# Optimization experiments

Hardware: AMD Instinct MI355X
Metric: run time of the kernel (lower is better)

The kernel has to match this reference:

```python
import jax, jax.numpy as jnp
import numpy as np

N_HEAD = 16


def setup_inputs() -> dict:
    key = jax.random.key(0)
    ks = jax.random.split(key, 10)
    B, S, D = 4, 2048, 1024
    inp = {
        "x": jax.random.normal(ks[0], (B, S, D), dtype=jnp.float32),
        "attention_mask": jnp.ones((B, S), dtype=jnp.int32),
        "Wq": jax.random.normal(ks[1], (D, D), dtype=jnp.float32) * 0.02,
        "bq": jax.random.normal(ks[2], (D,), dtype=jnp.float32) * 0.02,
        "Wk": jax.random.normal(ks[3], (D, D), dtype=jnp.float32) * 0.02,
        "bk": jax.random.normal(ks[4], (D,), dtype=jnp.float32) * 0.02,
        "Wv": jax.random.normal(ks[5], (D, D), dtype=jnp.float32) * 0.02,
        "bv": jax.random.normal(ks[6], (D,), dtype=jnp.float32) * 0.02,
        "Wp": jax.random.normal(ks[7], (D, D), dtype=jnp.float32) * 0.02,
        "bp": jax.random.normal(ks[8], (D,), dtype=jnp.float32) * 0.02,
    }
    return inp


def reference(x, attention_mask, Wq, bq, Wk, bk, Wv, bv, Wp, bp):
    B, S, D = x.shape
    H = N_HEAD
    HD = D // H
    scale = 1.0 / jnp.sqrt(jnp.asarray(HD, dtype=x.dtype))

    # q, kT, v projections -> (B, H, S, HD)
    q = (x @ Wq + bq).reshape(B, S, H, HD).transpose(0, 2, 1, 3)
    k = (x @ Wk + bk).reshape(B, S, H, HD).transpose(0, 2, 1, 3)
    v = (x @ Wv + bv).reshape(B, S, H, HD).transpose(0, 2, 1, 3)

    # scaled scores (B, H, S, S); dropout is identity at inference (p=0)
    logits = jnp.einsum("bhqd,bhkd->bhqk", q, k) * scale

    causal = jnp.tril(jnp.ones((S, S), dtype=bool))
    mask = causal[None, None, :, :] & attention_mask.astype(bool)[:, None, None, :]
    logits = jnp.where(mask, logits, -jnp.inf)

    attn_weights = jax.nn.softmax(logits, axis=-1)
    attn_weights = jnp.nan_to_num(attn_weights)  # fully-masked rows -> 0

    attn = jnp.einsum("bhqk,bhkd->bhqd", attn_weights, v)
    attn = attn.transpose(0, 2, 1, 3).reshape(B, S, D)  # (b h s hd) -> (b s D)
    return attn @ Wp + bp
```

## Files before the change

### kernel.cpp

```cpp
#include <hip/hip_runtime.h>
#include <stdint.h>

typedef __attribute__((ext_vector_type(8))) __bf16 bf16x8;
typedef __attribute__((ext_vector_type(4))) float f32x4;
typedef __attribute__((ext_vector_type(16))) float f32x16;
typedef __attribute__((ext_vector_type(8))) unsigned short u16x8;
typedef __attribute__((ext_vector_type(4))) unsigned int u32x4;
typedef unsigned short u16;

#define S_LEN 2048
#define DM 1024
#define NH 16
#define HD 64
#define BATCH 4

#define SWZ(r, b) ((b) ^ (((r)&7) << 4))

__device__ __forceinline__ int swz64(int row, int c16) {
  return ((row >> 1) << 7) + (((((row & 1) << 2) + c16) ^ ((row >> 1) & 7)) << 4);
}

__device__ __forceinline__ u16 f2b(float f) {
  union { float f; unsigned u; } v; v.f = f;
  unsigned u = v.u;
  u += 0x7fffu + ((u >> 16) & 1u);
  return (u16)(u >> 16);
}

__device__ __forceinline__ void gload_lds16(const void* g, void* l) {
  __builtin_amdgcn_global_load_lds((const __attribute__((address_space(1))) char*)g,
                                   (__attribute__((address_space(3))) char*)l, 16, 0, 0);
}


__global__ void cvt_x_kernel(const float* __restrict__ in, u16* __restrict__ out) {
  const int i = (blockIdx.x * 256 + threadIdx.x) * 8;
  const float4 a = *(const float4*)(in + i);
  const float4 b = *(const float4*)(in + i + 4);
  u16x8 o;
  o[0] = f2b(a.x); o[1] = f2b(a.y); o[2] = f2b(a.z); o[3] = f2b(a.w);
  o[4] = f2b(b.x); o[5] = f2b(b.y); o[6] = f2b(b.z); o[7] = f2b(b.w);
  *(u16x8*)(out + i) = o;
}

__global__ void transpose_cvt_w4_kernel(const float* __restrict__ Wq, const float* __restrict__ Wk,
                                        const float* __restrict__ Wv, const float* __restrict__ Wp,
                                        u16* __restrict__ WtQKV, u16* __restrict__ Wpt) {
  __shared__ float tile[64][65];
  const int z = blockIdx.z;
  const float* W = (z == 0) ? Wq : (z == 1) ? Wk : (z == 2) ? Wv : Wp;
  u16* Wt = (z == 3) ? Wpt : WtQKV + (size_t)z * 1048576;
  const int bx = blockIdx.x, by = blockIdx.y;
  const int t = threadIdx.x;
  const int r = t >> 6, c = t & 63;
#pragma unroll
  for (int i = 0; i < 64; i += 4)
    tile[r + i][c] = W[(size_t)(by * 64 + r + i) * DM + bx * 64 + c];
  __syncthreads();
#pragma unroll
  for (int i = 0; i < 64; i += 4)
    Wt[(size_t)(bx * 64 + r + i) * DM + by * 64 + c] = f2b(tile[c][r + i]);
}

__global__ void transpose_v_kernel(const u16* __restrict__ V, u16* __restrict__ Vt) {
  __shared__ u16 tile[64][68];
  const int st = blockIdx.x, bh = blockIdx.y;
  const int t = threadIdx.x;
  const int r = t >> 6, c = t & 63;
  const u16* src = V + ((size_t)bh * S_LEN + st * 64) * HD;
#pragma unroll
  for (int i = 0; i < 64; i += 4)
    tile[r + i][c] = src[(r + i) * HD + c];
  __syncthreads();
  u16* dst = Vt + (size_t)bh * HD * S_LEN + st * 64;
#pragma unroll
  for (int i = 0; i < 64; i += 4)
    dst[(size_t)(r + i) * S_LEN + c] = tile[c][r + i];
}


__device__ __forceinline__ void gemm_core_128(const u16* __restrict__ Atile,
                                              const u16* __restrict__ Btile,
                                              const int K, u16* As, u16* Bs,
                                              f32x4 acc[4][4]) {
  const int t = threadIdx.x;
  const int wave = t >> 6, lane = t & 63;
  const int wr = wave >> 1, wc = wave & 1;
  const int lr = lane & 15, lg = lane >> 4;

  for (int kt = 0; kt < K; kt += 32) {
#pragma unroll
    for (int i = 0; i < 2; ++i) {
      const int chunk = i * 4 + wave;
      const int off = chunk * 1024 + lane * 16;
      const int row = off >> 6;
      const int colb = off & 63;
      gload_lds16((const char*)Atile + ((size_t)row * K + kt) * 2 + colb,
                  (char*)As + chunk * 1024);
      gload_lds16((const char*)Btile + ((size_t)row * K + kt) * 2 + colb,
                  (char*)Bs + chunk * 1024);
    }
    __syncthreads();
    bf16x8 af[4], bfr[4];
#pragma unroll
    for (int m = 0; m < 4; ++m)
      af[m] = *(const bf16x8*)&As[(wr * 64 + m * 16 + lr) * 32 + lg * 8];
#pragma unroll
    for (int n = 0; n < 4; ++n)
      bfr[n] = *(const bf16x8*)&Bs[(wc * 64 + n * 16 + lr) * 32 + lg * 8];
#pragma unroll
    for (int m = 0; m < 4; ++m)
#pragma unroll
      for (int n = 0; n < 4; ++n)
        acc[m][n] = __builtin_amdgcn_mfma_f32_16x16x32_bf16(af[m], bfr[n], acc[m][n], 0, 0, 0);
    __syncthreads();
  }
}


__global__ __launch_bounds__(512, 2) void gemm_qkv_kernel(
    const u16* __restrict__ xb, const u16* __restrict__ Wt,
    const float* __restrict__ bq, const float* __restrict__ bk, const float* __restrict__ bv,
    u16* __restrict__ Qb, u16* __restrict__ Kb, u16* __restrict__ Vb) {
  __shared__ alignas(16) char L[4][40960];

  const int bcol = (blockIdx.x & 7) * 384;
  const int brow = (blockIdx.x >> 3) * 256;

  const int t = threadIdx.x;
  const int wave = t >> 6, lane = t & 63;
  const int wr = wave >> 2, wc = wave & 3;
  const int lr = lane & 15, lg = lane >> 4;

  f32x4 acc[8][6];
  const f32x4 zf = {0.f, 0.f, 0.f, 0.f};
#pragma unroll
  for (int m = 0; m < 8; ++m)
#pragma unroll
    for (int n = 0; n < 6; ++n) acc[m][n] = zf;

  const char* const Ag = (const char*)xb + (size_t)brow * 2048;
  const char* const Bg = (const char*)Wt + (size_t)bcol * 2048;

  int srcA0, srcA1, srcB0, srcB1, srcB2;
  {
    auto inv = [&](int p) {
      const int rp = p >> 7, slot = (p >> 4) & 7;
      const int v = slot ^ (rp & 7);
      const int row = rp * 2 + (v >> 2), c16 = v & 3;
      return row * 2048 + c16 * 16;
    };
    srcA0 = inv(t * 16);
    srcA1 = inv(8192 + t * 16);
    srcB0 = inv(t * 16);
    srcB1 = inv(8192 + t * 16);
    srcB2 = inv(16384 + t * 16);
  }

  const int aoff0 = swz64(wr * 128 + lr, lg);
  const int boff0 = swz64(wc * 96 + lr, lg);

  auto stage = [&](int kt, int b) {
    char* const base = &L[b][0];
    const int ko = kt * 64;
    gload_lds16(Ag + srcA0 + ko, base + t * 16);
    gload_lds16(Ag + srcA1 + ko, base + 8192 + t * 16);
    gload_lds16(Bg + srcB0 + ko, base + 16384 + t * 16);
    gload_lds16(Bg + srcB1 + ko, base + 24576 + t * 16);
    gload_lds16(Bg + srcB2 + ko, base + 32768 + t * 16);
  };

  const int NT = 32;
  stage(0, 0);
  stage(1, 1);
  for (int kt = 0; kt < NT; ++kt) {
    if (kt + 2 < NT) {
      stage(kt + 2, (kt + 2) & 3);
      asm volatile("s_waitcnt vmcnt(5)" ::: "memory");
    } else if (kt + 1 < NT) {
      asm volatile("s_waitcnt vmcnt(5)" ::: "memory");
    } else {
      asm volatile("s_waitcnt vmcnt(0)" ::: "memory");
    }
    asm volatile("s_barrier" ::: "memory");

    const char* const la = &L[kt & 3][0];
    const char* const lb = la + 16384;
    bf16x8 bf[6];
#pragma unroll
    for (int n = 0; n < 6; ++n) bf[n] = *(const bf16x8*)(lb + boff0 + n * 1024);
    __builtin_amdgcn_s_setprio(1);
#pragma unroll
    for (int m = 0; m < 8; ++m) {
      const bf16x8 af = *(const bf16x8*)(la + aoff0 + m * 1024);
#pragma unroll
      for (int n = 0; n < 6; ++n)
        acc[m][n] = __builtin_amdgcn_mfma_f32_16x16x32_bf16(af, bf[n], acc[m][n], 0, 0, 0);
    }
    __builtin_amdgcn_s_setprio(0);
  }

  const float qsc = 0.18033688011112042f;
#pragma unroll
  for (int m = 0; m < 8; ++m)
#pragma unroll
    for (int n = 0; n < 6; ++n) {
      const int colg = bcol + wc * 96 + n * 16 + lr;
      const int which = colg >> 10;
      const int c1 = colg & 1023;
      const float bias = (which == 0) ? bq[c1] : (which == 1) ? bk[c1] : bv[c1];
      u16* const dst = (which == 0) ? Qb : (which == 1) ? Kb : Vb;
#pragma unroll
      for (int j = 0; j < 4; ++j) {
        const int grow = brow + wr * 128 + m * 16 + lg * 4 + j;
        float val = acc[m][n][j] + bias;
        if (which == 0) val *= qsc;
        const int b = grow >> 11, s = grow & 2047;
        dst[(((size_t)b * NH + (c1 >> 6)) * S_LEN + s) * HD + (c1 & 63)] = f2b(val);
      }
    }
}

__global__ __launch_bounds__(256, 2) void gemm_out_kernel(
    const u16* __restrict__ A, const u16* __restrict__ Bt,
    const float* __restrict__ bias, float* __restrict__ out) {
  __shared__ alignas(16) u16 As[128 * 32], Bs[128 * 32];
  const int brow = blockIdx.x * 128;
  const int bcol = blockIdx.y * 128;
  f32x4 acc[4][4];
  const f32x4 zf = {0.f, 0.f, 0.f, 0.f};
#pragma unroll
  for (int m = 0; m < 4; ++m)
#pragma unroll
    for (int n = 0; n < 4; ++n) acc[m][n] = zf;

  gemm_core_128(A + (size_t)brow * DM, Bt + (size_t)bcol * DM, DM, As, Bs, acc);

  const int t = threadIdx.x, wave = t >> 6, lane = t & 63;
  const int wr = wave >> 1, wc = wave & 1, lr = lane & 15, lg = lane >> 4;
#pragma unroll
  for (int m = 0; m < 4; ++m)
#pragma unroll
    for (int n = 0; n < 4; ++n)
#pragma unroll
      for (int j = 0; j < 4; ++j) {
        const int grow = brow + wr * 64 + m * 16 + lg * 4 + j;
        const int col = bcol + wc * 64 + n * 16 + lr;
        out[(size_t)grow * DM + col] = acc[m][n][j] + bias[col];
      }
}


__global__ __launch_bounds__(256, 4) void flash2_kernel(
    const u16* __restrict__ Qb, const u16* __restrict__ Kb,
    const u16* __restrict__ Vt, u16* __restrict__ attn) {
  __shared__ alignas(16) u16 Ks[2][64 * 64];
  __shared__ alignas(16) u16 Vs[2][64 * 64];
  __shared__ float lbb[4][32];

  const int idx = blockIdx.x;
  const int c = idx & 255, r = idx >> 8;
  const int bh = (c & 15) * 4 + r;
  const int u = c >> 4;
  int qt;
  switch (r) {
    case 0: qt = u; break;
    case 1: qt = 15 - u; break;
    case 2: qt = (u + 8) & 15; break;
    default: qt = (7 - u) & 15; break;
  }

  const int t = threadIdx.x, wave = t >> 6, lane = t & 63;
  const int l31 = lane & 31, hi = lane >> 5;
  const int swz0 = (l31 & 7) << 4;
  const int b = bh >> 4, h = bh & 15;

  const char* kb0 = (const char*)(Kb + (size_t)bh * S_LEN * HD);
  const char* vb0 = (const char*)(Vt + (size_t)bh * HD * S_LEN);

  auto stage = [&](int kt, int bsel) {
#pragma unroll
    for (int i = 0; i < 2; ++i) {
      const int chunk = i * 4 + wave;
      const int off = chunk * 1024 + lane * 16;
      const int row = off >> 7, colb = off & 127;
      gload_lds16(kb0 + (size_t)kt * 8192 + row * 128 + SWZ(row, colb),
                  (char*)Ks[bsel] + chunk * 1024);
      gload_lds16(vb0 + (size_t)row * 4096 + kt * 128 + SWZ(row, colb),
                  (char*)Vs[bsel] + chunk * 1024);
    }
  };

  const int wq = qt * 128 + wave * 32;
  const int myq = wq + l31;

  const u16* qrow = Qb + ((size_t)bh * S_LEN + myq) * HD;
  bf16x8 qf[4];
#pragma unroll
  for (int ks = 0; ks < 4; ++ks)
    qf[ks] = *(const bf16x8*)(qrow + ks * 16 + hi * 8);

  f32x16 oa0, oa1;
#pragma unroll
  for (int r2 = 0; r2 < 16; ++r2) { oa0[r2] = 0.f; oa1[r2] = 0.f; }
  float lsum = 0.f;

  const int last = 2 * qt + 1;
  const int wlast = 2 * qt + (wave >> 1);

  stage(0, 0);
  int cur = 0;
  for (int kt = 0; kt <= last; ++kt) {
    __syncthreads();
    if (kt < last) stage(kt + 1, cur ^ 1);
    if (kt <= wlast) {
      f32x16 s0, s1;
#pragma unroll
      for (int r2 = 0; r2 < 16; ++r2) { s0[r2] = 0.f; s1[r2] = 0.f; }
      const char* ksb = (const char*)Ks[cur];
      __builtin_amdgcn_s_setprio(1);
#pragma unroll
      for (int ks = 0; ks < 4; ++ks) {
        const int byte0 = 32 * ks + 16 * hi;
        const bf16x8 ka = *(const bf16x8*)(ksb + l31 * 128 + (byte0 ^ swz0));
        const bf16x8 kb2 = *(const bf16x8*)(ksb + (32 + l31) * 128 + (byte0 ^ swz0));
        s0 = __builtin_amdgcn_mfma_f32_32x32x16_bf16(ka, qf[ks], s0, 0, 0, 0);
        s1 = __builtin_amdgcn_mfma_f32_32x32x16_bf16(kb2, qf[ks], s1, 0, 0, 0);
      }
      __builtin_amdgcn_s_setprio(0);

      if (kt == wlast) {
        const int kb4 = kt * 64 + 4 * hi;
#pragma unroll
        for (int r2 = 0; r2 < 16; ++r2) {
          const int key = kb4 + (r2 & 3) + 8 * (r2 >> 2);
          if (key > myq) s0[r2] = -1e30f;
          if (key + 32 > myq) s1[r2] = -1e30f;
        }
      }

#pragma unroll
      for (int r2 = 0; r2 < 16; ++r2) {
        s0[r2] = __builtin_amdgcn_exp2f(s0[r2]);
        s1[r2] = __builtin_amdgcn_exp2f(s1[r2]);
      }
      float q0 = (s0[0] + s0[1]) + (s0[2] + s0[3]);
      float q1 = (s0[4] + s0[5]) + (s0[6] + s0[7]);
      float q2 = (s0[8] + s0[9]) + (s0[10] + s0[11]);
      float q3 = (s0[12] + s0[13]) + (s0[14] + s0[15]);
      float q4 = (s1[0] + s1[1]) + (s1[2] + s1[3]);
      float q5 = (s1[4] + s1[5]) + (s1[6] + s1[7]);
      float q6 = (s1[8] + s1[9]) + (s1[10] + s1[11]);
      float q7 = (s1[12] + s1[13]) + (s1[14] + s1[15]);
      float rs = ((q0 + q1) + (q2 + q3)) + ((q4 + q5) + (q6 + q7));
      rs += __shfl_xor(rs, 32);
      lsum += rs;

      bf16x8 paf[4];
#pragma unroll
      for (int gg = 0; gg < 2; ++gg) {
        unsigned Wd[8];
#pragma unroll
        for (int k = 0; k < 8; ++k) {
          float lo = gg ? s1[2 * k] : s0[2 * k];
          float hi2 = gg ? s1[2 * k + 1] : s0[2 * k + 1];
          asm("v_cvt_pk_bf16_f32 %0, %1, %2" : "=v"(Wd[k]) : "v"(lo), "v"(hi2));
        }
#pragma unroll
        for (int hh = 0; hh < 2; ++hh) {
          unsigned a0 = Wd[4 * hh + 0], b0 = Wd[4 * hh + 2];
          unsigned a1 = Wd[4 * hh + 1], b1 = Wd[4 * hh + 3];
          asm("v_permlane32_swap_b32 %0, %1" : "+v"(a0), "+v"(b0));
          asm("v_permlane32_swap_b32 %0, %1" : "+v"(a1), "+v"(b1));
          u32x4 pw = {a0, a1, b0, b1};
          paf[2 * gg + hh] = __builtin_bit_cast(bf16x8, pw);
        }
      }

      const char* vsb = (const char*)Vs[cur];
      __builtin_amdgcn_s_setprio(1);
#pragma unroll
      for (int ks = 0; ks < 4; ++ks) {
        const int byte0 = 32 * ks + 16 * hi;
        const bf16x8 v0 = *(const bf16x8*)(vsb + l31 * 128 + (byte0 ^ swz0));
        const bf16x8 v1 = *(const bf16x8*)(vsb + (32 + l31) * 128 + (byte0 ^ swz0));
        oa0 = __builtin_amdgcn_mfma_f32_32x32x16_bf16(paf[ks], v0, oa0, 0, 0, 0);
        oa1 = __builtin_amdgcn_mfma_f32_32x32x16_bf16(paf[ks], v1, oa1, 0, 0, 0);
      }
      __builtin_amdgcn_s_setprio(0);
    }
    cur ^= 1;
  }

  if (hi == 0) lbb[wave][l31] = 1.0f / lsum;
#pragma unroll
  for (int r2 = 0; r2 < 16; ++r2) {
    const int cr = (r2 & 3) + 8 * (r2 >> 2) + 4 * hi;
    const int q = wq + cr;
    const float inv = lbb[wave][cr];
    u16* orow = attn + (((size_t)b * S_LEN + q) * NH + h) * HD;
    orow[l31] = f2b(oa0[r2] * inv);
    orow[32 + l31] = f2b(oa1[r2] * inv);
  }
}


extern "C" void kernel_launch(void* const* d_in, const int* in_sizes, int n_in,
                              void* d_out, int out_size, void* d_ws, size_t ws_size,
                              hipStream_t stream) {
  const float* x  = (const float*)d_in[0];
  const float* Wq = (const float*)d_in[2];
  const float* bq = (const float*)d_in[3];
  const float* Wk = (const float*)d_in[4];
  const float* bk = (const float*)d_in[5];
  const float* Wv = (const float*)d_in[6];
  const float* bv = (const float*)d_in[7];
  const float* Wp = (const float*)d_in[8];
  const float* bp = (const float*)d_in[9];

  char* ws = (char*)d_ws;
  u16* xb    = (u16*)(ws + 0);
  u16* WtQKV = (u16*)(ws + 16777216);
  u16* Wpt   = (u16*)(ws + 23068672);
  u16* Qb    = (u16*)(ws + 25165824);
  u16* Kb    = (u16*)(ws + 41943040);
  u16* Vb    = (u16*)(ws + 58720256);
  u16* Vtb   = (u16*)(ws + 75497472);
  u16* attnb = xb;

  cvt_x_kernel<<<4096, 256, 0, stream>>>(x, xb);
  transpose_cvt_w4_kernel<<<dim3(16, 16, 4), 256, 0, stream>>>(Wq, Wk, Wv, Wp, WtQKV, Wpt);

  gemm_qkv_kernel<<<dim3(256), 512, 0, stream>>>(xb, WtQKV, bq, bk, bv, Qb, Kb, Vb);
  transpose_v_kernel<<<dim3(32, 64), 256, 0, stream>>>(Vb, Vtb);
  flash2_kernel<<<dim3(1024), 256, 0, stream>>>(Qb, Kb, Vtb, attnb);
  gemm_out_kernel<<<dim3(64, 8), 256, 0, stream>>>(attnb, Wpt, bp, (float*)d_out);
}
```

Baseline: 158.7 us.

## Double per-wave query rows in flash attention to reuse K/V tiles

Each wave now handles 64 query rows (two 32-row groups) instead of 32, so each block covers 256 queries and the grid halves to 512 blocks. Every K and V fragment read from LDS feeds twice as many MFMAs, and each K/V tile is staged from global memory half as often overall. The block-to-(head, query-tile) mapping is reworked to pair light and heavy causal tiles. Register pressure roughly doubles for accumulators, so launch bounds drop to 2 blocks per SM, which lowers occupancy and coarsens load balance across the causal triangle.

```diff
diff --git a/kernel.cpp b/kernel.cpp
--- a/kernel.cpp
+++ b/kernel.cpp
@@ -251,32 +251,44 @@
 }
 
 
-__global__ __launch_bounds__(256, 4) void flash2_kernel(
+__global__ __launch_bounds__(256, 2) void flash2_kernel(
     const u16* __restrict__ Qb, const u16* __restrict__ Kb,
     const u16* __restrict__ Vt, u16* __restrict__ attn) {
   __shared__ alignas(16) u16 Ks[2][64 * 64];
   __shared__ alignas(16) u16 Vs[2][64 * 64];
-  __shared__ float lbb[4][32];
+  __shared__ float lbb[4][2][32];
 
   const int idx = blockIdx.x;
   const int c = idx & 255, r = idx >> 8;
-  const int bh = (c & 15) * 4 + r;
-  const int u = c >> 4;
-  int qt;
-  switch (r) {
-    case 0: qt = u; break;
-    case 1: qt = 15 - u; break;
-    case 2: qt = (u + 8) & 15; break;
-    default: qt = (7 - u) & 15; break;
-  }
+  const int x = c & 7, m = c >> 3;
+  const int bh = x * 8 + (m & 7);
+  const int u = m >> 3;
+  const int qb = r ? (7 - u) : u;
 
   const int t = threadIdx.x, wave = t >> 6, lane = t & 63;
   const int l31 = lane & 31, hi = lane >> 5;
   const int swz0 = (l31 & 7) << 4;
   const int b = bh >> 4, h = bh & 15;
 
+  const int wq = qb * 256 + wave * 64;
+  const int myqA = wq + l31, myqB = wq + 32 + l31;
+
   const char* kb0 = (const char*)(Kb + (size_t)bh * S_LEN * HD);
   const char* vb0 = (const char*)(Vt + (size_t)bh * HD * S_LEN);
+
+  const u16* qrowA = Qb + ((size_t)bh * S_LEN + myqA) * HD;
+  const u16* qrowB = Qb + ((size_t)bh * S_LEN + myqB) * HD;
+  bf16x8 qfA[4], qfB[4];
+#pragma unroll
+  for (int ks = 0; ks < 4; ++ks) {
+    qfA[ks] = *(const bf16x8*)(qrowA + ks * 16 + hi * 8);
+    qfB[ks] = *(const bf16x8*)(qrowB + ks * 16 + hi * 8);
+  }
+
+  f32x16 oaA0, oaA1, oaB0, oaB1;
+#pragma unroll
+  for (int r2 = 0; r2 < 16; ++r2) { oaA0[r2] = 0.f; oaA1[r2] = 0.f; oaB0[r2] = 0.f; oaB1[r2] = 0.f; }
+  float lsumA = 0.f, lsumB = 0.f;
 
   auto stage = [&](int kt, int bsel) {
 #pragma unroll
@@ -291,22 +303,8 @@
     }
   };
 
-  const int wq = qt * 128 + wave * 32;
-  const int myq = wq + l31;
-
-  const u16* qrow = Qb + ((size_t)bh * S_LEN + myq) * HD;
-  bf16x8 qf[4];
-#pragma unroll
-  for (int ks = 0; ks < 4; ++ks)
-    qf[ks] = *(const bf16x8*)(qrow + ks * 16 + hi * 8);
-
-  f32x16 oa0, oa1;
-#pragma unroll
-  for (int r2 = 0; r2 < 16; ++r2) { oa0[r2] = 0.f; oa1[r2] = 0.f; }
-  float lsum = 0.f;
-
-  const int last = 2 * qt + 1;
-  const int wlast = 2 * qt + (wave >> 1);
+  const int last = 4 * qb + 3;
+  const int wlast = 4 * qb + wave;
 
   stage(0, 0);
   int cur = 0;
@@ -314,9 +312,9 @@
     __syncthreads();
     if (kt < last) stage(kt + 1, cur ^ 1);
     if (kt <= wlast) {
-      f32x16 s0, s1;
-#pragma unroll
-      for (int r2 = 0; r2 < 16; ++r2) { s0[r2] = 0.f; s1[r2] = 0.f; }
+      f32x16 sA0, sA1, sB0, sB1;
+#pragma unroll
+      for (int r2 = 0; r2 < 16; ++r2) { sA0[r2] = 0.f; sA1[r2] = 0.f; sB0[r2] = 0.f; sB1[r2] = 0.f; }
       const char* ksb = (const char*)Ks[cur];
       __builtin_amdgcn_s_setprio(1);
 #pragma unroll
@@ -324,8 +322,10 @@
         const int byte0 = 32 * ks + 16 * hi;
         const bf16x8 ka = *(const bf16x8*)(ksb + l31 * 128 + (byte0 ^ swz0));
         const bf16x8 kb2 = *(const bf16x8*)(ksb + (32 + l31) * 128 + (byte0 ^ swz0));
-        s0 = __builtin_amdgcn_mfma_f32_32x32x16_bf16(ka, qf[ks], s0, 0, 0, 0);
-        s1 = __builtin_amdgcn_mfma_f32_32x32x16_bf16(kb2, qf[ks], s1, 0, 0, 0);
+        sA0 = __builtin_amdgcn_mfma_f32_32x32x16_bf16(ka, qfA[ks], sA0, 0, 0, 0);
+        sA1 = __builtin_amdgcn_mfma_f32_32x32x16_bf16(kb2, qfA[ks], sA1, 0, 0, 0);
+        sB0 = __builtin_amdgcn_mfma_f32_32x32x16_bf16(ka, qfB[ks], sB0, 0, 0, 0);
+        sB1 = __builtin_amdgcn_mfma_f32_32x32x16_bf16(kb2, qfB[ks], sB1, 0, 0, 0);
       }
       __builtin_amdgcn_s_setprio(0);
 
@@ -334,46 +334,68 @@
 #pragma unroll
         for (int r2 = 0; r2 < 16; ++r2) {
           const int key = kb4 + (r2 & 3) + 8 * (r2 >> 2);
-          if (key > myq) s0[r2] = -1e30f;
-          if (key + 32 > myq) s1[r2] = -1e30f;
+          if (key > myqA) sA0[r2] = -1e30f;
+          if (key + 32 > myqA) sA1[r2] = -1e30f;
+          if (key > myqB) sB0[r2] = -1e30f;
+          if (key + 32 > myqB) sB1[r2] = -1e30f;
         }
       }
 
 #pragma unroll
       for (int r2 = 0; r2 < 16; ++r2) {
-        s0[r2] = __builtin_amdgcn_exp2f(s0[r2]);
-        s1[r2] = __builtin_amdgcn_exp2f(s1[r2]);
-      }
-      float q0 = (s0[0] + s0[1]) + (s0[2] + s0[3]);
-      float q1 = (s0[4] + s0[5]) + (s0[6] + s0[7]);
-      float q2 = (s0[8] + s0[9]) + (s0[10] + s0[11]);
-      float q3 = (s0[12] + s0[13]) + (s0[14] + s0[15]);
-      float q4 = (s1[0] + s1[1]) + (s1[2] + s1[3]);
-      float q5 = (s1[4] + s1[5]) + (s1[6] + s1[7]);
-      float q6 = (s1[8] + s1[9]) + (s1[10] + s1[11]);
-      float q7 = (s1[12] + s1[13]) + (s1[14] + s1[15]);
-      float rs = ((q0 + q1) + (q2 + q3)) + ((q4 + q5) + (q6 + q7));
-      rs += __shfl_xor(rs, 32);
-      lsum += rs;
-
-      bf16x8 paf[4];
-#pragma unroll
-      for (int gg = 0; gg < 2; ++gg) {
-        unsigned Wd[8];
-#pragma unroll
-        for (int k = 0; k < 8; ++k) {
-          float lo = gg ? s1[2 * k] : s0[2 * k];
-          float hi2 = gg ? s1[2 * k + 1] : s0[2 * k + 1];
-          asm("v_cvt_pk_bf16_f32 %0, %1, %2" : "=v"(Wd[k]) : "v"(lo), "v"(hi2));
-        }
-#pragma unroll
-        for (int hh = 0; hh < 2; ++hh) {
-          unsigned a0 = Wd[4 * hh + 0], b0 = Wd[4 * hh + 2];
-          unsigned a1 = Wd[4 * hh + 1], b1 = Wd[4 * hh + 3];
-          asm("v_permlane32_swap_b32 %0, %1" : "+v"(a0), "+v"(b0));
-          asm("v_permlane32_swap_b32 %0, %1" : "+v"(a1), "+v"(b1));
-          u32x4 pw = {a0, a1, b0, b1};
-          paf[2 * gg + hh] = __builtin_bit_cast(bf16x8, pw);
+        sA0[r2] = __builtin_amdgcn_exp2f(sA0[r2]);
+        sA1[r2] = __builtin_amdgcn_exp2f(sA1[r2]);
+        sB0[r2] = __builtin_amdgcn_exp2f(sB0[r2]);
+        sB1[r2] = __builtin_amdgcn_exp2f(sB1[r2]);
+      }
+      {
+        float a0 = (sA0[0] + sA0[1]) + (sA0[2] + sA0[3]);
+        float a1 = (sA0[4] + sA0[5]) + (sA0[6] + sA0[7]);
+        float a2 = (sA0[8] + sA0[9]) + (sA0[10] + sA0[11]);
+        float a3 = (sA0[12] + sA0[13]) + (sA0[14] + sA0[15]);
+        float a4 = (sA1[0] + sA1[1]) + (sA1[2] + sA1[3]);
+        float a5 = (sA1[4] + sA1[5]) + (sA1[6] + sA1[7]);
+        float a6 = (sA1[8] + sA1[9]) + (sA1[10] + sA1[11]);
+        float a7 = (sA1[12] + sA1[13]) + (sA1[14] + sA1[15]);
+        float rsA = ((a0 + a1) + (a2 + a3)) + ((a4 + a5) + (a6 + a7));
+        rsA += __shfl_xor(rsA, 32);
+        lsumA += rsA;
+        float b0 = (sB0[0] + sB0[1]) + (sB0[2] + sB0[3]);
+        float b1 = (sB0[4] + sB0[5]) + (sB0[6] + sB0[7]);
+        float b2 = (sB0[8] + sB0[9]) + (sB0[10] + sB0[11]);
+        float b3 = (sB0[12] + sB0[13]) + (sB0[14] + sB0[15]);
+        float b4 = (sB1[0] + sB1[1]) + (sB1[2] + sB1[3]);
+        float b5 = (sB1[4] + sB1[5]) + (sB1[6] + sB1[7]);
+        float b6 = (sB1[8] + sB1[9]) + (sB1[10] + sB1[11]);
+        float b7 = (sB1[12] + sB1[13]) + (sB1[14] + sB1[15]);
+        float rsB = ((b0 + b1) + (b2 + b3)) + ((b4 + b5) + (b6 + b7));
+        rsB += __shfl_xor(rsB, 32);
+        lsumB += rsB;
+      }
+
+      bf16x8 pafA[4], pafB[4];
+#pragma unroll
+      for (int grp = 0; grp < 2; ++grp) {
+#pragma unroll
+        for (int gg = 0; gg < 2; ++gg) {
+          unsigned Wd[8];
+#pragma unroll
+          for (int k = 0; k < 8; ++k) {
+            float lo, hi2;
+            if (grp == 0) { lo = gg ? sA1[2 * k] : sA0[2 * k]; hi2 = gg ? sA1[2 * k + 1] : sA0[2 * k + 1]; }
+            else          { lo = gg ? sB1[2 * k] : sB0[2 * k]; hi2 = gg ? sB1[2 * k + 1] : sB0[2 * k + 1]; }
+            asm("v_cvt_pk_bf16_f32 %0, %1, %2" : "=v"(Wd[k]) : "v"(lo), "v"(hi2));
+          }
+#pragma unroll
+          for (int hh = 0; hh < 2; ++hh) {
+            unsigned a0 = Wd[4 * hh + 0], b0 = Wd[4 * hh + 2];
+            unsigned a1 = Wd[4 * hh + 1], b1 = Wd[4 * hh + 3];
+            asm("v_permlane32_swap_b32 %0, %1" : "+v"(a0), "+v"(b0));
+            asm("v_permlane32_swap_b32 %0, %1" : "+v"(a1), "+v"(b1));
+            u32x4 pw = {a0, a1, b0, b1};
+            if (grp == 0) pafA[2 * gg + hh] = __builtin_bit_cast(bf16x8, pw);
+            else          pafB[2 * gg + hh] = __builtin_bit_cast(bf16x8, pw);
+          }
         }
       }
 
@@ -384,23 +406,31 @@
         const int byte0 = 32 * ks + 16 * hi;
         const bf16x8 v0 = *(const bf16x8*)(vsb + l31 * 128 + (byte0 ^ swz0));
         const bf16x8 v1 = *(const bf16x8*)(vsb + (32 + l31) * 128 + (byte0 ^ swz0));
-        oa0 = __builtin_amdgcn_mfma_f32_32x32x16_bf16(paf[ks], v0, oa0, 0, 0, 0);
-        oa1 = __builtin_amdgcn_mfma_f32_32x32x16_bf16(paf[ks], v1, oa1, 0, 0, 0);
+        oaA0 = __builtin_amdgcn_mfma_f32_32x32x16_bf16(pafA[ks], v0, oaA0, 0, 0, 0);
+        oaA1 = __builtin_amdgcn_mfma_f32_32x32x16_bf16(pafA[ks], v1, oaA1, 0, 0, 0);
+        oaB0 = __builtin_amdgcn_mfma_f32_32x32x16_bf16(pafB[ks], v0, oaB0, 0, 0, 0);
+        oaB1 = __builtin_amdgcn_mfma_f32_32x32x16_bf16(pafB[ks], v1, oaB1, 0, 0, 0);
       }
       __builtin_amdgcn_s_setprio(0);
     }
     cur ^= 1;
   }
 
-  if (hi == 0) lbb[wave][l31] = 1.0f / lsum;
+  if (hi == 0) {
+    lbb[wave][0][l31] = 1.0f / lsumA;
+    lbb[wave][1][l31] = 1.0f / lsumB;
+  }
 #pragma unroll
   for (int r2 = 0; r2 < 16; ++r2) {
     const int cr = (r2 & 3) + 8 * (r2 >> 2) + 4 * hi;
-    const int q = wq + cr;
-    const float inv = lbb[wave][cr];
-    u16* orow = attn + (((size_t)b * S_LEN + q) * NH + h) * HD;
-    orow[l31] = f2b(oa0[r2] * inv);
-    orow[32 + l31] = f2b(oa1[r2] * inv);
+    const float invA = lbb[wave][0][cr];
+    const float invB = lbb[wave][1][cr];
+    u16* orowA = attn + (((size_t)b * S_LEN + (wq + cr)) * NH + h) * HD;
+    u16* orowB = attn + (((size_t)b * S_LEN + (wq + 32 + cr)) * NH + h) * HD;
+    orowA[l31] = f2b(oaA0[r2] * invA);
+    orowA[32 + l31] = f2b(oaA1[r2] * invA);
+    orowB[l31] = f2b(oaB0[r2] * invB);
+    orowB[32 + l31] = f2b(oaB1[r2] * invB);
   }
 }
 
@@ -433,6 +463,6 @@
 
   gemm_qkv_kernel<<<dim3(256), 512, 0, stream>>>(xb, WtQKV, bq, bk, bv, Qb, Kb, Vb);
   transpose_v_kernel<<<dim3(32, 64), 256, 0, stream>>>(Vb, Vtb);
-  flash2_kernel<<<dim3(1024), 256, 0, stream>>>(Qb, Kb, Vtb, attnb);
+  flash2_kernel<<<dim3(512), 256, 0, stream>>>(Qb, Kb, Vtb, attnb);
   gemm_out_kernel<<<dim3(64, 8), 256, 0, stream>>>(attnb, Wpt, bp, (float*)d_out);
 }
```

After: 158.5 us. About the same (-0.1%).

## Pipeline output GEMM with 4-buffer async LDS loads and merge prep kernels

Applied to the files above, without the earlier changes.

Rewrites the output projection GEMM to use 512-thread blocks with 128x256 tiles. It adds a 4-deep ring of LDS buffers filled by direct global-to-LDS loads two K-steps ahead, a swizzled LDS layout, a single barrier per step and raised wave priority around the MFMA block. The aim is to overlap global loads with matrix math and cut barrier stalls. It also folds the x conversion and the weight transpose/convert into one launch, saving a kernel launch. The prep path contains redundant leftover loop code that writes the first chunk twice.

```diff
diff --git a/kernel.cpp b/kernel.cpp
--- a/kernel.cpp
+++ b/kernel.cpp
@@ -33,25 +33,45 @@
 }
 
 
-__global__ void cvt_x_kernel(const float* __restrict__ in, u16* __restrict__ out) {
-  const int i = (blockIdx.x * 256 + threadIdx.x) * 8;
-  const float4 a = *(const float4*)(in + i);
-  const float4 b = *(const float4*)(in + i + 4);
-  u16x8 o;
-  o[0] = f2b(a.x); o[1] = f2b(a.y); o[2] = f2b(a.z); o[3] = f2b(a.w);
-  o[4] = f2b(b.x); o[5] = f2b(b.y); o[6] = f2b(b.z); o[7] = f2b(b.w);
-  *(u16x8*)(out + i) = o;
-}
-
-__global__ void transpose_cvt_w4_kernel(const float* __restrict__ Wq, const float* __restrict__ Wk,
-                                        const float* __restrict__ Wv, const float* __restrict__ Wp,
-                                        u16* __restrict__ WtQKV, u16* __restrict__ Wpt) {
+__global__ void prep_kernel(const float* __restrict__ x,
+                            const float* __restrict__ Wq, const float* __restrict__ Wk,
+                            const float* __restrict__ Wv, const float* __restrict__ Wp,
+                            u16* __restrict__ xb, u16* __restrict__ WtQKV,
+                            u16* __restrict__ Wpt) {
+  const int z = blockIdx.z;
+  const int t = threadIdx.x;
+  if (z == 4) {
+    const int bid = blockIdx.y * 16 + blockIdx.x;
+    int i = (bid * 256 + t) * 8;
+    for (int pass = 0; pass < 16; ++pass, i += 524288 * 8 / 8 * 8) {
+      const float4 a = *(const float4*)(x + i);
+      const float4 b = *(const float4*)(x + i + 4);
+      u16x8 o;
+      o[0] = f2b(a.x); o[1] = f2b(a.y); o[2] = f2b(a.z); o[3] = f2b(a.w);
+      o[4] = f2b(b.x); o[5] = f2b(b.y); o[6] = f2b(b.z); o[7] = f2b(b.w);
+      *(u16x8*)(xb + i) = o;
+      i += 524288 - 524288;
+      i = i - 8 + 524288;
+      i -= 524288 - 8;
+      i = i;
+      break;
+    }
+    int base = (bid * 256 + t) * 8;
+    for (int p = (base == i ? 0 : 0); p < 16; ++p) {
+      const int j = base + p * 524288;
+      const float4 a = *(const float4*)(x + j);
+      const float4 b = *(const float4*)(x + j + 4);
+      u16x8 o;
+      o[0] = f2b(a.x); o[1] = f2b(a.y); o[2] = f2b(a.z); o[3] = f2b(a.w);
+      o[4] = f2b(b.x); o[5] = f2b(b.y); o[6] = f2b(b.z); o[7] = f2b(b.w);
+      *(u16x8*)(xb + j) = o;
+    }
+    return;
+  }
   __shared__ float tile[64][65];
-  const int z = blockIdx.z;
   const float* W = (z == 0) ? Wq : (z == 1) ? Wk : (z == 2) ? Wv : Wp;
   u16* Wt = (z == 3) ? Wpt : WtQKV + (size_t)z * 1048576;
   const int bx = blockIdx.x, by = blockIdx.y;
-  const int t = threadIdx.x;
   const int r = t >> 6, c = t & 63;
 #pragma unroll
   for (int i = 0; i < 64; i += 4)
@@ -76,45 +96,6 @@
 #pragma unroll
   for (int i = 0; i < 64; i += 4)
     dst[(size_t)(r + i) * S_LEN + c] = tile[c][r + i];
-}
-
-
-__device__ __forceinline__ void gemm_core_128(const u16* __restrict__ Atile,
-                                              const u16* __restrict__ Btile,
-                                              const int K, u16* As, u16* Bs,
-                                              f32x4 acc[4][4]) {
-  const int t = threadIdx.x;
-  const int wave = t >> 6, lane = t & 63;
-  const int wr = wave >> 1, wc = wave & 1;
-  const int lr = lane & 15, lg = lane >> 4;
-
-  for (int kt = 0; kt < K; kt += 32) {
-#pragma unroll
-    for (int i = 0; i < 2; ++i) {
-      const int chunk = i * 4 + wave;
-      const int off = chunk * 1024 + lane * 16;
-      const int row = off >> 6;
-      const int colb = off & 63;
-      gload_lds16((const char*)Atile + ((size_t)row * K + kt) * 2 + colb,
-                  (char*)As + chunk * 1024);
-      gload_lds16((const char*)Btile + ((size_t)row * K + kt) * 2 + colb,
-                  (char*)Bs + chunk * 1024);
-    }
-    __syncthreads();
-    bf16x8 af[4], bfr[4];
-#pragma unroll
-    for (int m = 0; m < 4; ++m)
-      af[m] = *(const bf16x8*)&As[(wr * 64 + m * 16 + lr) * 32 + lg * 8];
-#pragma unroll
-    for (int n = 0; n < 4; ++n)
-      bfr[n] = *(const bf16x8*)&Bs[(wc * 64 + n * 16 + lr) * 32 + lg * 8];
-#pragma unroll
-    for (int m = 0; m < 4; ++m)
-#pragma unroll
-      for (int n = 0; n < 4; ++n)
-        acc[m][n] = __builtin_amdgcn_mfma_f32_16x16x32_bf16(af[m], bfr[n], acc[m][n], 0, 0, 0);
-    __syncthreads();
-  }
 }
 
 
@@ -221,12 +202,21 @@
     }
 }
 
-__global__ __launch_bounds__(256, 2) void gemm_out_kernel(
+
+__global__ __launch_bounds__(512, 2) void gemm_out_kernel(
     const u16* __restrict__ A, const u16* __restrict__ Bt,
     const float* __restrict__ bias, float* __restrict__ out) {
-  __shared__ alignas(16) u16 As[128 * 32], Bs[128 * 32];
-  const int brow = blockIdx.x * 128;
-  const int bcol = blockIdx.y * 128;
+  __shared__ alignas(16) char L[4][24576];
+
+  const int c = blockIdx.x & 7, mm = blockIdx.x >> 3;
+  const int bcol = (c >> 1) * 256;
+  const int brow = ((c & 1) * 32 + mm) * 128;
+
+  const int t = threadIdx.x;
+  const int wave = t >> 6, lane = t & 63;
+  const int wr = wave >> 2, wc = wave & 3;
+  const int lr = lane & 15, lg = lane >> 4;
+
   f32x4 acc[4][4];
   const f32x4 zf = {0.f, 0.f, 0.f, 0.f};
 #pragma unroll
@@ -234,10 +224,63 @@
 #pragma unroll
     for (int n = 0; n < 4; ++n) acc[m][n] = zf;
 
-  gemm_core_128(A + (size_t)brow * DM, Bt + (size_t)bcol * DM, DM, As, Bs, acc);
-
-  const int t = threadIdx.x, wave = t >> 6, lane = t & 63;
-  const int wr = wave >> 1, wc = wave & 1, lr = lane & 15, lg = lane >> 4;
+  const char* const Ag = (const char*)A + (size_t)brow * 2048;
+  const char* const Bg = (const char*)Bt + (size_t)bcol * 2048;
+
+  int srcA0, srcB0, srcB1;
+  {
+    auto inv = [&](int p) {
+      const int rp = p >> 7, slot = (p >> 4) & 7;
+      const int v = slot ^ (rp & 7);
+      const int row = rp * 2 + (v >> 2), c16 = v & 3;
+      return row * 2048 + c16 * 16;
+    };
+    srcA0 = inv(t * 16);
+    srcB0 = inv(t * 16);
+    srcB1 = inv(8192 + t * 16);
+  }
+
+  const int aoff0 = swz64(wr * 64 + lr, lg);
+  const int boff0 = swz64(wc * 64 + lr, lg);
+
+  auto stage = [&](int kt, int b) {
+    char* const base = &L[b][0];
+    const int ko = kt * 64;
+    gload_lds16(Ag + srcA0 + ko, base + t * 16);
+    gload_lds16(Bg + srcB0 + ko, base + 8192 + t * 16);
+    gload_lds16(Bg + srcB1 + ko, base + 16384 + t * 16);
+  };
+
+  const int NT = 32;
+  stage(0, 0);
+  stage(1, 1);
+  for (int kt = 0; kt < NT; ++kt) {
+    if (kt + 2 < NT) {
+      stage(kt + 2, (kt + 2) & 3);
+      asm volatile("s_waitcnt vmcnt(3)" ::: "memory");
+    } else if (kt + 1 < NT) {
+      asm volatile("s_waitcnt vmcnt(3)" ::: "memory");
+    } else {
+      asm volatile("s_waitcnt vmcnt(0)" ::: "memory");
+    }
+    asm volatile("s_barrier" ::: "memory");
+
+    const char* const la = &L[kt & 3][0];
+    const char* const lb = la + 8192;
+    bf16x8 bf[4];
+#pragma unroll
+    for (int n = 0; n < 4; ++n) bf[n] = *(const bf16x8*)(lb + boff0 + n * 1024);
+    __builtin_amdgcn_s_setprio(1);
+#pragma unroll
+    for (int m = 0; m < 4; ++m) {
+      const bf16x8 af = *(const bf16x8*)(la + aoff0 + m * 1024);
+#pragma unroll
+      for (int n = 0; n < 4; ++n)
+        acc[m][n] = __builtin_amdgcn_mfma_f32_16x16x32_bf16(af, bf[n], acc[m][n], 0, 0, 0);
+    }
+    __builtin_amdgcn_s_setprio(0);
+  }
+
 #pragma unroll
   for (int m = 0; m < 4; ++m)
 #pragma unroll
@@ -428,11 +471,10 @@
   u16* Vtb   = (u16*)(ws + 75497472);
   u16* attnb = xb;
 
-  cvt_x_kernel<<<4096, 256, 0, stream>>>(x, xb);
-  transpose_cvt_w4_kernel<<<dim3(16, 16, 4), 256, 0, stream>>>(Wq, Wk, Wv, Wp, WtQKV, Wpt);
+  prep_kernel<<<dim3(16, 16, 5), 256, 0, stream>>>(x, Wq, Wk, Wv, Wp, xb, WtQKV, Wpt);
 
   gemm_qkv_kernel<<<dim3(256), 512, 0, stream>>>(xb, WtQKV, bq, bk, bv, Qb, Kb, Vb);
   transpose_v_kernel<<<dim3(32, 64), 256, 0, stream>>>(Vb, Vtb);
   flash2_kernel<<<dim3(1024), 256, 0, stream>>>(Qb, Kb, Vtb, attnb);
-  gemm_out_kernel<<<dim3(64, 8), 256, 0, stream>>>(attnb, Wpt, bp, (float*)d_out);
-}
+  gemm_out_kernel<<<dim3(256), 512, 0, stream>>>(attnb, Wpt, bp, (float*)d_out);
+}
```

After: 155.9 us. Within noise of the previous version (-1.8%).
